# Performance work log

Hardware: AMD Instinct MI355X
Metric: run time of the kernel (lower is better)

Reference implementation:

```python
import jax, jax.numpy as jnp
import numpy as np

N = 2048  # num_neurons == batch == input/hidden/output size (required for shape consistency)


def setup_inputs() -> dict:
    key = jax.random.key(0)
    ks = jax.random.split(key, 8)
    s = 1.0 / np.sqrt(N)
    return {
        "x": jax.random.normal(ks[0], (N, N), jnp.float32),
        "W1": jax.random.normal(ks[1], (N, N), jnp.float32) * s,
        "b1": jnp.zeros((N,), jnp.float32),
        "W2": jax.random.normal(ks[2], (N, N), jnp.float32) * s,
        "b2": jnp.zeros((N,), jnp.float32),
        "W3": jax.random.normal(ks[3], (N, N), jnp.float32) * s,
        "b3": jnp.zeros((N,), jnp.float32),
        "weights": jax.random.uniform(ks[4], (N, N), jnp.float32) * 2.0 - 1.0,
        "last_spike_time": jax.random.uniform(ks[5], (N,), jnp.float32) * 10.0,
        "membrane_potential": jnp.zeros((N,), jnp.float32),
        "n": jnp.zeros((N,), jnp.float32),
        "m": jnp.zeros((N,), jnp.float32),
        "h": jnp.zeros((N,), jnp.float32),
    }


def reference(x, W1, b1, W2, b2, W3, b3, weights, last_spike_time,
              membrane_potential, n, m, h):
    dt = 0.01
    membrane_decay = 0.5
    current_time = 10.0
    # --- Hodgkin-Huxley style dynamics (elementwise chain) ---
    v = membrane_decay * membrane_potential + jax.nn.sigmoid(x @ W1.T + b1)  # [B,N]
    spiking = v > 1.0
    v = jnp.where(spiking, 0.0, v)
    alpha_n = 0.01 * (v + 55.0) / (1.0 - jnp.exp(-(v + 55.0) / 10.0))
    beta_n = 0.125 * jnp.exp(-(v + 65.0) / 80.0)
    alpha_m = 0.1 * (v + 40.0) / (1.0 - jnp.exp(-(v + 40.0) / 10.0))
    beta_m = 4.0 * jnp.exp(-(v + 65.0) / 18.0)
    alpha_h = 0.07 * jnp.exp(-(v + 65.0) / 20.0)
    beta_h = 1.0 / (1.0 + jnp.exp(-(v + 35.0) / 10.0))
    n_new = n + dt * (alpha_n * (1.0 - n) - beta_n * n)  # [B,N]
    m_new = m + dt * (alpha_m * (1.0 - m) - beta_m * m)
    h_new = h + dt * (alpha_h * (1.0 - h) - beta_h * h)
    # --- all-pairs STDP update (vectorized form of the O(n^2) Python loop) ---
    tau_plus, tau_minus = 15.0, 25.0
    A_plus, A_minus = 0.02, 0.015
    row_spiked = jnp.any(spiking, axis=1)                 # [B] == spiking_neurons[i].any()
    pair_mask = row_spiked[:, None] | row_spiked[None, :]  # [B,B]
    ts = current_time - last_spike_time                   # [N] (B == N)
    dt_mat = ts[:, None] - ts[None, :]                    # delta_t for every pair
    dw = jnp.where(dt_mat > 0,
                   -A_minus * jnp.exp(-jnp.abs(dt_mat) / tau_minus),
                   A_plus * jnp.exp(-jnp.abs(dt_mat) / tau_plus))
    new_weights = jnp.clip(weights + jnp.where(pair_mask, dw, 0.0), -1.0, 1.0)
    # --- output MLP ---
    out = jax.nn.sigmoid(jax.nn.sigmoid(v @ W2.T + b2) @ W3.T + b3)  # [B,output]
    return out, new_weights, n_new, m_new, h_new
```

## Files before the change

### kernel.cpp

```cpp
#include <hip/hip_runtime.h>
#include <hip/hip_bf16.h>
#include <math.h>


#define NN 2048
#define BK 64
#define KHALF (NN / 2)
#define KTH (KHALF / BK)
#define NT (NN / 128)

typedef __attribute__((ext_vector_type(8))) short bf16x8;
typedef __attribute__((ext_vector_type(4))) float f32x4;
typedef __attribute__((ext_vector_type(4))) short s16x4;

__device__ __forceinline__ short f2bf(float f) {
    union { float f; unsigned u; } a; a.f = f;
    unsigned r = a.u + 0x7FFFu + ((a.u >> 16) & 1u);
    return (short)(r >> 16);
}

__device__ __forceinline__ float bf2f(short s) {
    union { unsigned u; float f; } a;
    a.u = ((unsigned)(unsigned short)s) << 16;
    return a.f;
}

__device__ __forceinline__ void gload16(const short* g, short* l) {
    __builtin_amdgcn_global_load_lds(
        (const __attribute__((address_space(1))) unsigned int*)g,
        (__attribute__((address_space(3))) unsigned int*)l, 16, 0, 0);
}

__device__ __forceinline__ float sigmoidf_(float x) {
    return 1.0f / (1.0f + expf(-x));
}

__global__ void conv3_kernel(const float* __restrict__ s0, const float* __restrict__ s1,
                             const float* __restrict__ s2,
                             short* __restrict__ d0, short* __restrict__ d1,
                             short* __restrict__ d2, int* __restrict__ flags)
{
    const float* src; short* dst;
    if      (blockIdx.y == 0) { src = s0; dst = d0; }
    else if (blockIdx.y == 1) { src = s1; dst = d1; }
    else                      { src = s2; dst = d2; }
    int i = blockIdx.x * blockDim.x + threadIdx.x;
    float4 v = reinterpret_cast<const float4*>(src)[i];
    s16x4 o;
    o.x = f2bf(v.x); o.y = f2bf(v.y); o.z = f2bf(v.z); o.w = f2bf(v.w);
    reinterpret_cast<s16x4*>(dst)[i] = o;
    if (blockIdx.y == 0 && blockIdx.x < NN / 256)
        flags[blockIdx.x * blockDim.x + threadIdx.x] = 0;
}

__global__ void conv1_kernel(const float* __restrict__ src, short* __restrict__ dst) {
    int i = blockIdx.x * blockDim.x + threadIdx.x;
    float4 v = reinterpret_cast<const float4*>(src)[i];
    s16x4 o;
    o.x = f2bf(v.x); o.y = f2bf(v.y); o.z = f2bf(v.z); o.w = f2bf(v.w);
    reinterpret_cast<s16x4*>(dst)[i] = o;
}

__global__ __launch_bounds__(512) void gemm_partial(
    const short* __restrict__ A, const short* __restrict__ B,
    short* __restrict__ P)
{
    __shared__ short As[2][128 * BK] __attribute__((aligned(16)));
    __shared__ short Bs[2][128 * BK] __attribute__((aligned(16)));

    const int tid  = threadIdx.x;
    const int lane = tid & 63;
    const int wid  = tid >> 6;
    const int row0 = blockIdx.y * 128;
    const int col0 = blockIdx.x * 128;
    const int kbase = blockIdx.z * KHALF;
    const int wm   = (wid >> 2) * 64;
    const int wn   = (wid & 3) * 32;
    const int lrow = lane & 15;
    const int lk16 = (lane >> 4) << 3;

    f32x4 acc[4][2] = {};

    auto stage = [&](int buf, int k0) {
#pragma unroll
        for (int s = 0; s < 2; ++s) {
            int c = tid + s * 512;
            int r = c >> 3;
            int ksrc = ((c & 7) ^ (r & 7)) << 3;
            gload16(A + (size_t)(row0 + r) * NN + k0 + ksrc, &As[buf][c * 8]);
            gload16(B + (size_t)(col0 + r) * NN + k0 + ksrc, &Bs[buf][c * 8]);
        }
    };

    auto compute = [&](int buf) {
        bf16x8 af[4][2], bfv[2][2];
#pragma unroll
        for (int i = 0; i < 4; ++i) {
            const int row = wm + i * 16 + lrow;
#pragma unroll
            for (int kk = 0; kk < 2; ++kk) {
                const int ke = (lk16 + kk * 32) ^ ((row & 7) << 3);
                af[i][kk] = *reinterpret_cast<const bf16x8*>(&As[buf][row * BK + ke]);
            }
        }
#pragma unroll
        for (int j = 0; j < 2; ++j) {
            const int row = wn + j * 16 + lrow;
#pragma unroll
            for (int kk = 0; kk < 2; ++kk) {
                const int ke = (lk16 + kk * 32) ^ ((row & 7) << 3);
                bfv[j][kk] = *reinterpret_cast<const bf16x8*>(&Bs[buf][row * BK + ke]);
            }
        }
#pragma unroll
        for (int kk = 0; kk < 2; ++kk)
#pragma unroll
            for (int i = 0; i < 4; ++i)
#pragma unroll
                for (int j = 0; j < 2; ++j)
                    acc[i][j] = __builtin_amdgcn_mfma_f32_16x16x32_bf16(
                        af[i][kk], bfv[j][kk], acc[i][j], 0, 0, 0);
    };

    stage(0, kbase);
    __syncthreads();
    int cur = 0;
    for (int t = 0; t < KTH - 1; ++t) {
        stage(cur ^ 1, kbase + (t + 1) * BK);
        compute(cur);
        __syncthreads();
        cur ^= 1;
    }
    compute(cur);

    short* outp = P + (size_t)blockIdx.z * NN * NN;
#pragma unroll
    for (int i = 0; i < 4; ++i) {
#pragma unroll
        for (int j = 0; j < 2; ++j) {
            const int gcol = col0 + wn + j * 16 + lrow;
#pragma unroll
            for (int r = 0; r < 4; ++r) {
                const int grow = row0 + wm + i * 16 + ((lane >> 4) << 2) + r;
                outp[(size_t)grow * NN + gcol] = f2bf(acc[i][j][r]);
            }
        }
    }
}

template <int EPI>
__global__ void combine_kernel(
    const short* __restrict__ p0, const short* __restrict__ p1,
    const float* __restrict__ bias,
    const float* __restrict__ mp,
    const float* __restrict__ n_in, const float* __restrict__ m_in,
    const float* __restrict__ h_in,
    short* __restrict__ out_bf, float* __restrict__ out_f,
    float* __restrict__ out_n, float* __restrict__ out_m,
    float* __restrict__ out_h,
    int* __restrict__ flags)
{
    int idx = blockIdx.x * blockDim.x + threadIdx.x;
    int row = idx >> 9;
    int g   = idx & 511;
    s16x4 a = reinterpret_cast<const s16x4*>(p0)[idx];
    s16x4 b = reinterpret_cast<const s16x4*>(p1)[idx];
    float4 bi = reinterpret_cast<const float4*>(bias)[g];
    float pre[4] = { bf2f(a.x) + bf2f(b.x) + bi.x,
                     bf2f(a.y) + bf2f(b.y) + bi.y,
                     bf2f(a.z) + bf2f(b.z) + bi.z,
                     bf2f(a.w) + bf2f(b.w) + bi.w };
    if constexpr (EPI == 1) {
        float4 mp4 = reinterpret_cast<const float4*>(mp)[g];
        float4 n4  = reinterpret_cast<const float4*>(n_in)[g];
        float4 m4  = reinterpret_cast<const float4*>(m_in)[g];
        float4 h4  = reinterpret_cast<const float4*>(h_in)[g];
        float mpv[4] = {mp4.x, mp4.y, mp4.z, mp4.w};
        float nv[4]  = {n4.x, n4.y, n4.z, n4.w};
        float mv[4]  = {m4.x, m4.y, m4.z, m4.w};
        float hv[4]  = {h4.x, h4.y, h4.z, h4.w};
        s16x4 vb;
        float on[4], om[4], oh[4];
#pragma unroll
        for (int t = 0; t < 4; ++t) {
            float v = 0.5f * mpv[t] + sigmoidf_(pre[t]);
            if (v > 1.0f) { flags[row] = 1; v = 0.0f; }
            vb[t] = f2bf(v);
            float an = 0.01f * (v + 55.0f) / (1.0f - expf(-(v + 55.0f) / 10.0f));
            float bn = 0.125f * expf(-(v + 65.0f) / 80.0f);
            float am = 0.1f  * (v + 40.0f) / (1.0f - expf(-(v + 40.0f) / 10.0f));
            float bm = 4.0f  * expf(-(v + 65.0f) / 18.0f);
            float ah = 0.07f * expf(-(v + 65.0f) / 20.0f);
            float bh = 1.0f  / (1.0f + expf(-(v + 35.0f) / 10.0f));
            on[t] = nv[t] + 0.01f * (an * (1.0f - nv[t]) - bn * nv[t]);
            om[t] = mv[t] + 0.01f * (am * (1.0f - mv[t]) - bm * mv[t]);
            oh[t] = hv[t] + 0.01f * (ah * (1.0f - hv[t]) - bh * hv[t]);
        }
        reinterpret_cast<s16x4*>(out_bf)[idx] = vb;
        reinterpret_cast<float4*>(out_n)[idx] = make_float4(on[0], on[1], on[2], on[3]);
        reinterpret_cast<float4*>(out_m)[idx] = make_float4(om[0], om[1], om[2], om[3]);
        reinterpret_cast<float4*>(out_h)[idx] = make_float4(oh[0], oh[1], oh[2], oh[3]);
    } else if constexpr (EPI == 2) {
        s16x4 o;
        o.x = f2bf(sigmoidf_(pre[0])); o.y = f2bf(sigmoidf_(pre[1]));
        o.z = f2bf(sigmoidf_(pre[2])); o.w = f2bf(sigmoidf_(pre[3]));
        reinterpret_cast<s16x4*>(out_bf)[idx] = o;
    } else {
        reinterpret_cast<float4*>(out_f)[idx] =
            make_float4(sigmoidf_(pre[0]), sigmoidf_(pre[1]),
                        sigmoidf_(pre[2]), sigmoidf_(pre[3]));
    }
}

__global__ void stdp_kernel(const float* __restrict__ w, const float* __restrict__ lst,
                            const int* __restrict__ flags, float* __restrict__ outw)
{
    int idx = blockIdx.x * blockDim.x + threadIdx.x;
    int i  = idx >> 9;
    int j4 = (idx & 511) << 2;
    float4 wv = reinterpret_cast<const float4*>(w)[idx];
    float o[4] = {wv.x, wv.y, wv.z, wv.w};
    const int   rsi = flags[i];
    const float tsi = 10.0f - lst[i];
#pragma unroll
    for (int t = 0; t < 4; ++t) {
        int j = j4 + t;
        if (rsi | flags[j]) {
            float dtm = tsi - (10.0f - lst[j]);
            float dw = (dtm > 0.0f) ? (-0.015f * expf(-fabsf(dtm) / 25.0f))
                                    : ( 0.02f  * expf(-fabsf(dtm) / 15.0f));
            o[t] += dw;
        }
        o[t] = fminf(1.0f, fmaxf(-1.0f, o[t]));
    }
    float4 ov = make_float4(o[0], o[1], o[2], o[3]);
    reinterpret_cast<float4*>(outw)[idx] = ov;
}

extern "C" void kernel_launch(void* const* d_in, const int* in_sizes, int n_in,
                              void* d_out, int out_size, void* d_ws, size_t ws_size,
                              hipStream_t stream)
{
    const float* x   = (const float*)d_in[0];
    const float* W1  = (const float*)d_in[1];
    const float* b1  = (const float*)d_in[2];
    const float* W2  = (const float*)d_in[3];
    const float* b2  = (const float*)d_in[4];
    const float* W3  = (const float*)d_in[5];
    const float* b3  = (const float*)d_in[6];
    const float* wts = (const float*)d_in[7];
    const float* lst = (const float*)d_in[8];
    const float* mp  = (const float*)d_in[9];
    const float* nin = (const float*)d_in[10];
    const float* min_ = (const float*)d_in[11];
    const float* hin = (const float*)d_in[12];

    const size_t NSQ = (size_t)NN * NN;
    float* out    = (float*)d_out;
    float* out_w  = out + NSQ;
    float* out_n  = out + 2 * NSQ;
    float* out_m  = out + 3 * NSQ;
    float* out_h  = out + 4 * NSQ;

    short* R1 = (short*)d_ws;
    short* R2 = R1 + NSQ;
    short* R3 = R2 + NSQ;
    short* R4 = R3 + NSQ;
    short* P  = R4 + NSQ;
    int* flags = (int*)(P + 2 * NSQ);

    const int convBlocks = (int)(NSQ / 4 / 256);

    conv3_kernel<<<dim3(convBlocks, 3), 256, 0, stream>>>(x, W1, W2, R1, R2, R4, flags);

    dim3 grid(NT, NT, 2);
    gemm_partial<<<grid, 512, 0, stream>>>(R1, R2, P);
    conv1_kernel<<<convBlocks, 256, 0, stream>>>(W3, R1);
    combine_kernel<1><<<convBlocks, 256, 0, stream>>>(P, P + NSQ, b1, mp, nin, min_, hin,
                                                      R3, nullptr, out_n, out_m, out_h, flags);
    stdp_kernel<<<convBlocks, 256, 0, stream>>>(wts, lst, flags, out_w);
    gemm_partial<<<grid, 512, 0, stream>>>(R3, R4, P);
    combine_kernel<2><<<convBlocks, 256, 0, stream>>>(P, P + NSQ, b2, nullptr, nullptr, nullptr,
                                                      nullptr, R2, nullptr, nullptr, nullptr,
                                                      nullptr, nullptr);
    gemm_partial<<<grid, 512, 0, stream>>>(R2, R1, P);
    combine_kernel<3><<<convBlocks, 256, 0, stream>>>(P, P + NSQ, b3, nullptr, nullptr, nullptr,
                                                      nullptr, nullptr, out, nullptr, nullptr,
                                                      nullptr, nullptr);
}
```

Before: 133.9 us.

## Split GEMM K four ways, single-buffer LDS, and reuse fewer workspace buffers

Each GEMM now splits K into four slices instead of two, which doubles the grid to 1024 blocks for more parallelism. To fit more blocks per CU, the LDS double-buffering is removed and launch bounds request higher occupancy. The combine kernels sum four bf16 partials, so partial-buffer traffic and bf16 rounding error both grow. Workspace is cut to two bf16 matrices plus four partials, with the W2 and W3 conversions moved between stages. This also adds serialization, and load latency is no longer hidden by prefetching.

```diff
diff --git a/kernel.cpp b/kernel.cpp
--- a/kernel.cpp
+++ b/kernel.cpp
@@ -5,8 +5,8 @@
 
 #define NN 2048
 #define BK 64
-#define KHALF (NN / 2)
-#define KTH (KHALF / BK)
+#define KSLICE (NN / 4)
+#define KTQ (KSLICE / BK)
 #define NT (NN / 128)
 
 typedef __attribute__((ext_vector_type(8))) short bf16x8;
@@ -35,15 +35,12 @@
     return 1.0f / (1.0f + expf(-x));
 }
 
-__global__ void conv3_kernel(const float* __restrict__ s0, const float* __restrict__ s1,
-                             const float* __restrict__ s2,
+__global__ void conv2_kernel(const float* __restrict__ s0, const float* __restrict__ s1,
                              short* __restrict__ d0, short* __restrict__ d1,
-                             short* __restrict__ d2, int* __restrict__ flags)
-{
-    const float* src; short* dst;
-    if      (blockIdx.y == 0) { src = s0; dst = d0; }
-    else if (blockIdx.y == 1) { src = s1; dst = d1; }
-    else                      { src = s2; dst = d2; }
+                             int* __restrict__ flags)
+{
+    const float* src = (blockIdx.y == 0) ? s0 : s1;
+    short*       dst = (blockIdx.y == 0) ? d0 : d1;
     int i = blockIdx.x * blockDim.x + threadIdx.x;
     float4 v = reinterpret_cast<const float4*>(src)[i];
     s16x4 o;
@@ -61,19 +58,19 @@
     reinterpret_cast<s16x4*>(dst)[i] = o;
 }
 
-__global__ __launch_bounds__(512) void gemm_partial(
+__global__ __launch_bounds__(512, 8) void gemm_partial(
     const short* __restrict__ A, const short* __restrict__ B,
     short* __restrict__ P)
 {
-    __shared__ short As[2][128 * BK] __attribute__((aligned(16)));
-    __shared__ short Bs[2][128 * BK] __attribute__((aligned(16)));
+    __shared__ short As[128 * BK] __attribute__((aligned(16)));
+    __shared__ short Bs[128 * BK] __attribute__((aligned(16)));
 
     const int tid  = threadIdx.x;
     const int lane = tid & 63;
     const int wid  = tid >> 6;
     const int row0 = blockIdx.y * 128;
     const int col0 = blockIdx.x * 128;
-    const int kbase = blockIdx.z * KHALF;
+    const int kbase = blockIdx.z * KSLICE;
     const int wm   = (wid >> 2) * 64;
     const int wn   = (wid & 3) * 32;
     const int lrow = lane & 15;
@@ -81,18 +78,18 @@
 
     f32x4 acc[4][2] = {};
 
-    auto stage = [&](int buf, int k0) {
+    for (int t = 0; t < KTQ; ++t) {
+        const int k0 = kbase + t * BK;
 #pragma unroll
         for (int s = 0; s < 2; ++s) {
             int c = tid + s * 512;
             int r = c >> 3;
             int ksrc = ((c & 7) ^ (r & 7)) << 3;
-            gload16(A + (size_t)(row0 + r) * NN + k0 + ksrc, &As[buf][c * 8]);
-            gload16(B + (size_t)(col0 + r) * NN + k0 + ksrc, &Bs[buf][c * 8]);
-        }
-    };
-
-    auto compute = [&](int buf) {
+            gload16(A + (size_t)(row0 + r) * NN + k0 + ksrc, &As[c * 8]);
+            gload16(B + (size_t)(col0 + r) * NN + k0 + ksrc, &Bs[c * 8]);
+        }
+        __syncthreads();
+
         bf16x8 af[4][2], bfv[2][2];
 #pragma unroll
         for (int i = 0; i < 4; ++i) {
@@ -100,7 +97,7 @@
 #pragma unroll
             for (int kk = 0; kk < 2; ++kk) {
                 const int ke = (lk16 + kk * 32) ^ ((row & 7) << 3);
-                af[i][kk] = *reinterpret_cast<const bf16x8*>(&As[buf][row * BK + ke]);
+                af[i][kk] = *reinterpret_cast<const bf16x8*>(&As[row * BK + ke]);
             }
         }
 #pragma unroll
@@ -109,7 +106,7 @@
 #pragma unroll
             for (int kk = 0; kk < 2; ++kk) {
                 const int ke = (lk16 + kk * 32) ^ ((row & 7) << 3);
-                bfv[j][kk] = *reinterpret_cast<const bf16x8*>(&Bs[buf][row * BK + ke]);
+                bfv[j][kk] = *reinterpret_cast<const bf16x8*>(&Bs[row * BK + ke]);
             }
         }
 #pragma unroll
@@ -120,18 +117,8 @@
                 for (int j = 0; j < 2; ++j)
                     acc[i][j] = __builtin_amdgcn_mfma_f32_16x16x32_bf16(
                         af[i][kk], bfv[j][kk], acc[i][j], 0, 0, 0);
-    };
-
-    stage(0, kbase);
-    __syncthreads();
-    int cur = 0;
-    for (int t = 0; t < KTH - 1; ++t) {
-        stage(cur ^ 1, kbase + (t + 1) * BK);
-        compute(cur);
         __syncthreads();
-        cur ^= 1;
-    }
-    compute(cur);
+    }
 
     short* outp = P + (size_t)blockIdx.z * NN * NN;
 #pragma unroll
@@ -151,6 +138,7 @@
 template <int EPI>
 __global__ void combine_kernel(
     const short* __restrict__ p0, const short* __restrict__ p1,
+    const short* __restrict__ p2, const short* __restrict__ p3,
     const float* __restrict__ bias,
     const float* __restrict__ mp,
     const float* __restrict__ n_in, const float* __restrict__ m_in,
@@ -165,11 +153,13 @@
     int g   = idx & 511;
     s16x4 a = reinterpret_cast<const s16x4*>(p0)[idx];
     s16x4 b = reinterpret_cast<const s16x4*>(p1)[idx];
+    s16x4 c = reinterpret_cast<const s16x4*>(p2)[idx];
+    s16x4 d = reinterpret_cast<const s16x4*>(p3)[idx];
     float4 bi = reinterpret_cast<const float4*>(bias)[g];
-    float pre[4] = { bf2f(a.x) + bf2f(b.x) + bi.x,
-                     bf2f(a.y) + bf2f(b.y) + bi.y,
-                     bf2f(a.z) + bf2f(b.z) + bi.z,
-                     bf2f(a.w) + bf2f(b.w) + bi.w };
+    float pre[4] = { bf2f(a.x) + bf2f(b.x) + bf2f(c.x) + bf2f(d.x) + bi.x,
+                     bf2f(a.y) + bf2f(b.y) + bf2f(c.y) + bf2f(d.y) + bi.y,
+                     bf2f(a.z) + bf2f(b.z) + bf2f(c.z) + bf2f(d.z) + bi.z,
+                     bf2f(a.w) + bf2f(b.w) + bf2f(c.w) + bf2f(d.w) + bi.w };
     if constexpr (EPI == 1) {
         float4 mp4 = reinterpret_cast<const float4*>(mp)[g];
         float4 n4  = reinterpret_cast<const float4*>(n_in)[g];
@@ -262,29 +252,31 @@
     float* out_m  = out + 3 * NSQ;
     float* out_h  = out + 4 * NSQ;
 
-    short* R1 = (short*)d_ws;
-    short* R2 = R1 + NSQ;
-    short* R3 = R2 + NSQ;
-    short* R4 = R3 + NSQ;
-    short* P  = R4 + NSQ;
-    int* flags = (int*)(P + 2 * NSQ);
+    short* S0 = (short*)d_ws;
+    short* S1 = S0 + NSQ;
+    short* P  = S1 + NSQ;
+    int* flags = (int*)(P + 4 * NSQ);
 
     const int convBlocks = (int)(NSQ / 4 / 256);
 
-    conv3_kernel<<<dim3(convBlocks, 3), 256, 0, stream>>>(x, W1, W2, R1, R2, R4, flags);
-
-    dim3 grid(NT, NT, 2);
-    gemm_partial<<<grid, 512, 0, stream>>>(R1, R2, P);
-    conv1_kernel<<<convBlocks, 256, 0, stream>>>(W3, R1);
-    combine_kernel<1><<<convBlocks, 256, 0, stream>>>(P, P + NSQ, b1, mp, nin, min_, hin,
-                                                      R3, nullptr, out_n, out_m, out_h, flags);
+    conv2_kernel<<<dim3(convBlocks, 2), 256, 0, stream>>>(x, W1, S0, S1, flags);
+
+    dim3 grid(NT, NT, 4);
+    gemm_partial<<<grid, 512, 0, stream>>>(S0, S1, P);
+    conv1_kernel<<<convBlocks, 256, 0, stream>>>(W2, S1);
+    combine_kernel<1><<<convBlocks, 256, 0, stream>>>(P, P + NSQ, P + 2 * NSQ, P + 3 * NSQ,
+                                                      b1, mp, nin, min_, hin,
+                                                      S0, nullptr, out_n, out_m, out_h, flags);
     stdp_kernel<<<convBlocks, 256, 0, stream>>>(wts, lst, flags, out_w);
-    gemm_partial<<<grid, 512, 0, stream>>>(R3, R4, P);
-    combine_kernel<2><<<convBlocks, 256, 0, stream>>>(P, P + NSQ, b2, nullptr, nullptr, nullptr,
-                                                      nullptr, R2, nullptr, nullptr, nullptr,
-                                                      nullptr, nullptr);
-    gemm_partial<<<grid, 512, 0, stream>>>(R2, R1, P);
-    combine_kernel<3><<<convBlocks, 256, 0, stream>>>(P, P + NSQ, b3, nullptr, nullptr, nullptr,
-                                                      nullptr, nullptr, out, nullptr, nullptr,
-                                                      nullptr, nullptr);
-}
+    gemm_partial<<<grid, 512, 0, stream>>>(S0, S1, P);
+    combine_kernel<2><<<convBlocks, 256, 0, stream>>>(P, P + NSQ, P + 2 * NSQ, P + 3 * NSQ,
+                                                      b2, nullptr, nullptr, nullptr, nullptr,
+                                                      S1, nullptr, nullptr, nullptr, nullptr,
+                                                      nullptr);
+    conv1_kernel<<<convBlocks, 256, 0, stream>>>(W3, S0);
+    gemm_partial<<<grid, 512, 0, stream>>>(S1, S0, P);
+    combine_kernel<3><<<convBlocks, 256, 0, stream>>>(P, P + NSQ, P + 2 * NSQ, P + 3 * NSQ,
+                                                      b3, nullptr, nullptr, nullptr, nullptr,
+                                                      nullptr, out, nullptr, nullptr, nullptr,
+                                                      nullptr);
+}
```

New measurement: 154.5 us. 1.15x slower.

## Merge weight conversions and STDP update into GEMM/combine launches

Applied to the files above, without the earlier changes.

Removes separate launches by moving the W2 and W3 bf16 conversions into extra grid slices of the combine kernels, and runs the STDP weight update as a third z-slice of the second GEMM launch. The intent is to cut launch count and let bandwidth-bound work overlap with compute-bound GEMM tiles. The trade-offs are a larger GEMM grid, with the STDP blocks reserving the GEMM's LDS footprint, and possible tail imbalance.

```diff
diff --git a/kernel.cpp b/kernel.cpp
--- a/kernel.cpp
+++ b/kernel.cpp
@@ -35,39 +35,32 @@
     return 1.0f / (1.0f + expf(-x));
 }
 
-__global__ void conv3_kernel(const float* __restrict__ s0, const float* __restrict__ s1,
-                             const float* __restrict__ s2,
-                             short* __restrict__ d0, short* __restrict__ d1,
-                             short* __restrict__ d2, int* __restrict__ flags)
-{
-    const float* src; short* dst;
-    if      (blockIdx.y == 0) { src = s0; dst = d0; }
-    else if (blockIdx.y == 1) { src = s1; dst = d1; }
-    else                      { src = s2; dst = d2; }
-    int i = blockIdx.x * blockDim.x + threadIdx.x;
+__device__ __forceinline__ void conv_item(const float* __restrict__ src,
+                                          short* __restrict__ dst, int i) {
     float4 v = reinterpret_cast<const float4*>(src)[i];
     s16x4 o;
     o.x = f2bf(v.x); o.y = f2bf(v.y); o.z = f2bf(v.z); o.w = f2bf(v.w);
     reinterpret_cast<s16x4*>(dst)[i] = o;
-    if (blockIdx.y == 0 && blockIdx.x < NN / 256)
-        flags[blockIdx.x * blockDim.x + threadIdx.x] = 0;
-}
-
-__global__ void conv1_kernel(const float* __restrict__ src, short* __restrict__ dst) {
+}
+
+__global__ void conv2_kernel(const float* __restrict__ s0, const float* __restrict__ s1,
+                             short* __restrict__ d0, short* __restrict__ d1,
+                             int* __restrict__ flags)
+{
     int i = blockIdx.x * blockDim.x + threadIdx.x;
-    float4 v = reinterpret_cast<const float4*>(src)[i];
-    s16x4 o;
-    o.x = f2bf(v.x); o.y = f2bf(v.y); o.z = f2bf(v.z); o.w = f2bf(v.w);
-    reinterpret_cast<s16x4*>(dst)[i] = o;
-}
-
-__global__ __launch_bounds__(512) void gemm_partial(
+    if (blockIdx.y == 0) {
+        conv_item(s0, d0, i);
+        if (blockIdx.x < NN / 256)
+            flags[blockIdx.x * blockDim.x + threadIdx.x] = 0;
+    } else {
+        conv_item(s1, d1, i);
+    }
+}
+
+__device__ __forceinline__ void gemm_body(
     const short* __restrict__ A, const short* __restrict__ B,
-    short* __restrict__ P)
-{
-    __shared__ short As[2][128 * BK] __attribute__((aligned(16)));
-    __shared__ short Bs[2][128 * BK] __attribute__((aligned(16)));
-
+    short* __restrict__ P, short (*As)[128 * BK], short (*Bs)[128 * BK])
+{
     const int tid  = threadIdx.x;
     const int lane = tid & 63;
     const int wid  = tid >> 6;
@@ -148,19 +141,66 @@
     }
 }
 
-template <int EPI>
-__global__ void combine_kernel(
+__global__ __launch_bounds__(512) void gemm_partial(
+    const short* __restrict__ A, const short* __restrict__ B,
+    short* __restrict__ P)
+{
+    __shared__ short As[2][128 * BK] __attribute__((aligned(16)));
+    __shared__ short Bs[2][128 * BK] __attribute__((aligned(16)));
+    gemm_body(A, B, P, As, Bs);
+}
+
+__global__ __launch_bounds__(512) void gemm_stdp(
+    const short* __restrict__ A, const short* __restrict__ B,
+    short* __restrict__ P,
+    const float* __restrict__ w, const float* __restrict__ lst,
+    const int* __restrict__ flags, float* __restrict__ outw)
+{
+    __shared__ short As[2][128 * BK] __attribute__((aligned(16)));
+    __shared__ short Bs[2][128 * BK] __attribute__((aligned(16)));
+    if (blockIdx.z == 2) {
+        const int bflat = blockIdx.y * gridDim.x + blockIdx.x;
+#pragma unroll
+        for (int u = 0; u < 8; ++u) {
+            int idx = bflat * 4096 + u * 512 + threadIdx.x;
+            int i  = idx >> 9;
+            int j4 = (idx & 511) << 2;
+            float4 wv = reinterpret_cast<const float4*>(w)[idx];
+            float o[4] = {wv.x, wv.y, wv.z, wv.w};
+            const int   rsi = flags[i];
+            const float tsi = 10.0f - lst[i];
+#pragma unroll
+            for (int t = 0; t < 4; ++t) {
+                int j = j4 + t;
+                if (rsi | flags[j]) {
+                    float dtm = tsi - (10.0f - lst[j]);
+                    float dw = (dtm > 0.0f) ? (-0.015f * expf(-fabsf(dtm) / 25.0f))
+                                            : ( 0.02f  * expf(-fabsf(dtm) / 15.0f));
+                    o[t] += dw;
+                }
+                o[t] = fminf(1.0f, fmaxf(-1.0f, o[t]));
+            }
+            reinterpret_cast<float4*>(outw)[idx] = make_float4(o[0], o[1], o[2], o[3]);
+        }
+        return;
+    }
+    gemm_body(A, B, P, As, Bs);
+}
+
+__global__ void comb1_mix(
     const short* __restrict__ p0, const short* __restrict__ p1,
     const float* __restrict__ bias,
     const float* __restrict__ mp,
     const float* __restrict__ n_in, const float* __restrict__ m_in,
     const float* __restrict__ h_in,
-    short* __restrict__ out_bf, float* __restrict__ out_f,
+    short* __restrict__ out_v,
     float* __restrict__ out_n, float* __restrict__ out_m,
     float* __restrict__ out_h,
-    int* __restrict__ flags)
+    int* __restrict__ flags,
+    const float* __restrict__ convsrc, short* __restrict__ convdst)
 {
     int idx = blockIdx.x * blockDim.x + threadIdx.x;
+    if (blockIdx.y == 1) { conv_item(convsrc, convdst, idx); return; }
     int row = idx >> 9;
     int g   = idx & 511;
     s16x4 a = reinterpret_cast<const s16x4*>(p0)[idx];
@@ -170,71 +210,71 @@
                      bf2f(a.y) + bf2f(b.y) + bi.y,
                      bf2f(a.z) + bf2f(b.z) + bi.z,
                      bf2f(a.w) + bf2f(b.w) + bi.w };
-    if constexpr (EPI == 1) {
-        float4 mp4 = reinterpret_cast<const float4*>(mp)[g];
-        float4 n4  = reinterpret_cast<const float4*>(n_in)[g];
-        float4 m4  = reinterpret_cast<const float4*>(m_in)[g];
-        float4 h4  = reinterpret_cast<const float4*>(h_in)[g];
-        float mpv[4] = {mp4.x, mp4.y, mp4.z, mp4.w};
-        float nv[4]  = {n4.x, n4.y, n4.z, n4.w};
-        float mv[4]  = {m4.x, m4.y, m4.z, m4.w};
-        float hv[4]  = {h4.x, h4.y, h4.z, h4.w};
-        s16x4 vb;
-        float on[4], om[4], oh[4];
-#pragma unroll
-        for (int t = 0; t < 4; ++t) {
-            float v = 0.5f * mpv[t] + sigmoidf_(pre[t]);
-            if (v > 1.0f) { flags[row] = 1; v = 0.0f; }
-            vb[t] = f2bf(v);
-            float an = 0.01f * (v + 55.0f) / (1.0f - expf(-(v + 55.0f) / 10.0f));
-            float bn = 0.125f * expf(-(v + 65.0f) / 80.0f);
-            float am = 0.1f  * (v + 40.0f) / (1.0f - expf(-(v + 40.0f) / 10.0f));
-            float bm = 4.0f  * expf(-(v + 65.0f) / 18.0f);
-            float ah = 0.07f * expf(-(v + 65.0f) / 20.0f);
-            float bh = 1.0f  / (1.0f + expf(-(v + 35.0f) / 10.0f));
-            on[t] = nv[t] + 0.01f * (an * (1.0f - nv[t]) - bn * nv[t]);
-            om[t] = mv[t] + 0.01f * (am * (1.0f - mv[t]) - bm * mv[t]);
-            oh[t] = hv[t] + 0.01f * (ah * (1.0f - hv[t]) - bh * hv[t]);
-        }
-        reinterpret_cast<s16x4*>(out_bf)[idx] = vb;
-        reinterpret_cast<float4*>(out_n)[idx] = make_float4(on[0], on[1], on[2], on[3]);
-        reinterpret_cast<float4*>(out_m)[idx] = make_float4(om[0], om[1], om[2], om[3]);
-        reinterpret_cast<float4*>(out_h)[idx] = make_float4(oh[0], oh[1], oh[2], oh[3]);
-    } else if constexpr (EPI == 2) {
-        s16x4 o;
-        o.x = f2bf(sigmoidf_(pre[0])); o.y = f2bf(sigmoidf_(pre[1]));
-        o.z = f2bf(sigmoidf_(pre[2])); o.w = f2bf(sigmoidf_(pre[3]));
-        reinterpret_cast<s16x4*>(out_bf)[idx] = o;
-    } else {
-        reinterpret_cast<float4*>(out_f)[idx] =
-            make_float4(sigmoidf_(pre[0]), sigmoidf_(pre[1]),
-                        sigmoidf_(pre[2]), sigmoidf_(pre[3]));
-    }
-}
-
-__global__ void stdp_kernel(const float* __restrict__ w, const float* __restrict__ lst,
-                            const int* __restrict__ flags, float* __restrict__ outw)
+    float4 mp4 = reinterpret_cast<const float4*>(mp)[g];
+    float4 n4  = reinterpret_cast<const float4*>(n_in)[g];
+    float4 m4  = reinterpret_cast<const float4*>(m_in)[g];
+    float4 h4  = reinterpret_cast<const float4*>(h_in)[g];
+    float mpv[4] = {mp4.x, mp4.y, mp4.z, mp4.w};
+    float nv[4]  = {n4.x, n4.y, n4.z, n4.w};
+    float mv[4]  = {m4.x, m4.y, m4.z, m4.w};
+    float hv[4]  = {h4.x, h4.y, h4.z, h4.w};
+    s16x4 vb;
+    float on[4], om[4], oh[4];
+#pragma unroll
+    for (int t = 0; t < 4; ++t) {
+        float v = 0.5f * mpv[t] + sigmoidf_(pre[t]);
+        if (v > 1.0f) { flags[row] = 1; v = 0.0f; }
+        vb[t] = f2bf(v);
+        float an = 0.01f * (v + 55.0f) / (1.0f - expf(-(v + 55.0f) / 10.0f));
+        float bn = 0.125f * expf(-(v + 65.0f) / 80.0f);
+        float am = 0.1f  * (v + 40.0f) / (1.0f - expf(-(v + 40.0f) / 10.0f));
+        float bm = 4.0f  * expf(-(v + 65.0f) / 18.0f);
+        float ah = 0.07f * expf(-(v + 65.0f) / 20.0f);
+        float bh = 1.0f  / (1.0f + expf(-(v + 35.0f) / 10.0f));
+        on[t] = nv[t] + 0.01f * (an * (1.0f - nv[t]) - bn * nv[t]);
+        om[t] = mv[t] + 0.01f * (am * (1.0f - mv[t]) - bm * mv[t]);
+        oh[t] = hv[t] + 0.01f * (ah * (1.0f - hv[t]) - bh * hv[t]);
+    }
+    reinterpret_cast<s16x4*>(out_v)[idx] = vb;
+    reinterpret_cast<float4*>(out_n)[idx] = make_float4(on[0], on[1], on[2], on[3]);
+    reinterpret_cast<float4*>(out_m)[idx] = make_float4(om[0], om[1], om[2], om[3]);
+    reinterpret_cast<float4*>(out_h)[idx] = make_float4(oh[0], oh[1], oh[2], oh[3]);
+}
+
+__global__ void comb2_mix(
+    const short* __restrict__ p0, const short* __restrict__ p1,
+    const float* __restrict__ bias,
+    short* __restrict__ out_bf,
+    const float* __restrict__ convsrc, short* __restrict__ convdst)
 {
     int idx = blockIdx.x * blockDim.x + threadIdx.x;
-    int i  = idx >> 9;
-    int j4 = (idx & 511) << 2;
-    float4 wv = reinterpret_cast<const float4*>(w)[idx];
-    float o[4] = {wv.x, wv.y, wv.z, wv.w};
-    const int   rsi = flags[i];
-    const float tsi = 10.0f - lst[i];
-#pragma unroll
-    for (int t = 0; t < 4; ++t) {
-        int j = j4 + t;
-        if (rsi | flags[j]) {
-            float dtm = tsi - (10.0f - lst[j]);
-            float dw = (dtm > 0.0f) ? (-0.015f * expf(-fabsf(dtm) / 25.0f))
-                                    : ( 0.02f  * expf(-fabsf(dtm) / 15.0f));
-            o[t] += dw;
-        }
-        o[t] = fminf(1.0f, fmaxf(-1.0f, o[t]));
-    }
-    float4 ov = make_float4(o[0], o[1], o[2], o[3]);
-    reinterpret_cast<float4*>(outw)[idx] = ov;
+    if (blockIdx.y == 1) { conv_item(convsrc, convdst, idx); return; }
+    int g = idx & 511;
+    s16x4 a = reinterpret_cast<const s16x4*>(p0)[idx];
+    s16x4 b = reinterpret_cast<const s16x4*>(p1)[idx];
+    float4 bi = reinterpret_cast<const float4*>(bias)[g];
+    s16x4 o;
+    o.x = f2bf(sigmoidf_(bf2f(a.x) + bf2f(b.x) + bi.x));
+    o.y = f2bf(sigmoidf_(bf2f(a.y) + bf2f(b.y) + bi.y));
+    o.z = f2bf(sigmoidf_(bf2f(a.z) + bf2f(b.z) + bi.z));
+    o.w = f2bf(sigmoidf_(bf2f(a.w) + bf2f(b.w) + bi.w));
+    reinterpret_cast<s16x4*>(out_bf)[idx] = o;
+}
+
+__global__ void combine3(
+    const short* __restrict__ p0, const short* __restrict__ p1,
+    const float* __restrict__ bias, float* __restrict__ out_f)
+{
+    int idx = blockIdx.x * blockDim.x + threadIdx.x;
+    int g = idx & 511;
+    s16x4 a = reinterpret_cast<const s16x4*>(p0)[idx];
+    s16x4 b = reinterpret_cast<const s16x4*>(p1)[idx];
+    float4 bi = reinterpret_cast<const float4*>(bias)[g];
+    reinterpret_cast<float4*>(out_f)[idx] = make_float4(
+        sigmoidf_(bf2f(a.x) + bf2f(b.x) + bi.x),
+        sigmoidf_(bf2f(a.y) + bf2f(b.y) + bi.y),
+        sigmoidf_(bf2f(a.z) + bf2f(b.z) + bi.z),
+        sigmoidf_(bf2f(a.w) + bf2f(b.w) + bi.w));
 }
 
 extern "C" void kernel_launch(void* const* d_in, const int* in_sizes, int n_in,
@@ -271,20 +311,14 @@
 
     const int convBlocks = (int)(NSQ / 4 / 256);
 
-    conv3_kernel<<<dim3(convBlocks, 3), 256, 0, stream>>>(x, W1, W2, R1, R2, R4, flags);
-
-    dim3 grid(NT, NT, 2);
-    gemm_partial<<<grid, 512, 0, stream>>>(R1, R2, P);
-    conv1_kernel<<<convBlocks, 256, 0, stream>>>(W3, R1);
-    combine_kernel<1><<<convBlocks, 256, 0, stream>>>(P, P + NSQ, b1, mp, nin, min_, hin,
-                                                      R3, nullptr, out_n, out_m, out_h, flags);
-    stdp_kernel<<<convBlocks, 256, 0, stream>>>(wts, lst, flags, out_w);
-    gemm_partial<<<grid, 512, 0, stream>>>(R3, R4, P);
-    combine_kernel<2><<<convBlocks, 256, 0, stream>>>(P, P + NSQ, b2, nullptr, nullptr, nullptr,
-                                                      nullptr, R2, nullptr, nullptr, nullptr,
-                                                      nullptr, nullptr);
-    gemm_partial<<<grid, 512, 0, stream>>>(R2, R1, P);
-    combine_kernel<3><<<convBlocks, 256, 0, stream>>>(P, P + NSQ, b3, nullptr, nullptr, nullptr,
-                                                      nullptr, nullptr, out, nullptr, nullptr,
-                                                      nullptr, nullptr);
-}
+    conv2_kernel<<<dim3(convBlocks, 2), 256, 0, stream>>>(x, W1, R1, R2, flags);
+    gemm_partial<<<dim3(NT, NT, 2), 512, 0, stream>>>(R1, R2, P);
+    comb1_mix<<<dim3(convBlocks, 2), 256, 0, stream>>>(
+        P, P + NSQ, b1, mp, nin, min_, hin,
+        R3, out_n, out_m, out_h, flags, W2, R4);
+    gemm_stdp<<<dim3(NT, NT, 3), 512, 0, stream>>>(R3, R4, P, wts, lst, flags, out_w);
+    comb2_mix<<<dim3(convBlocks, 2), 256, 0, stream>>>(
+        P, P + NSQ, b2, R2, W3, R1);
+    gemm_partial<<<dim3(NT, NT, 2), 512, 0, stream>>>(R2, R1, P);
+    combine3<<<convBlocks, 256, 0, stream>>>(P, P + NSQ, b3, out);
+}
```

After: 123.7 us (median of 2 runs). 1.08x faster.
